# Kernel optimization log

Hardware: AMD Instinct MI355X
Metric: run time of the kernel (lower is better)

## Reference

```python
import jax, jax.numpy as jnp
import numpy as np

CRACK_VAL = 0.05  # intensity written along crack lines


def _crack_mask(endpoints, H, W):
    """Vectorized Bresenham rasterization.
    endpoints: [B, K, 4] int32 rows (y0, x0, y1, x1).
    Returns bool mask [B, 1, H, W] of pixels covered by any crack line.
    """
    B, K, _ = endpoints.shape
    ep = endpoints.reshape(-1, 4).astype(jnp.int32)  # [N=B*K, 4]
    y0, x0, y1, x1 = ep[:, 0], ep[:, 1], ep[:, 2], ep[:, 3]
    dx = jnp.abs(x1 - x0)
    dy = jnp.abs(y1 - y0)
    sx = jnp.where(x0 < x1, 1, -1).astype(jnp.int32)
    sy = jnp.where(y0 < y1, 1, -1).astype(jnp.int32)
    nsteps = jnp.maximum(dx, dy)  # line has nsteps+1 pixels
    T = max(H, W)  # static upper bound on line length

    def step(carry, t):
        cx, cy, err = carry
        valid = t <= nsteps  # pixel emitted this step is on the line
        rec = (cx, cy, valid)
        e2 = 2 * err
        cond_x = e2 > -dy
        cond_y = e2 < dx
        err = err - jnp.where(cond_x, dy, 0) + jnp.where(cond_y, dx, 0)
        cx = cx + jnp.where(cond_x, sx, 0)
        cy = cy + jnp.where(cond_y, sy, 0)
        return (cx, cy, err), rec

    init = (x0, y0, dx - dy)
    _, (cxs, cys, valids) = jax.lax.scan(step, init, jnp.arange(T, dtype=jnp.int32))
    # cxs/cys/valids: [T, N]
    bidx = jnp.broadcast_to(jnp.arange(B * K, dtype=jnp.int32) // K, cxs.shape)
    inb = (cys >= 0) & (cys < H) & (cxs >= 0) & (cxs < W)  # matches original bounds check
    ok = valids & inb
    flat = bidx * (H * W) + jnp.clip(cys, 0, H - 1) * W + jnp.clip(cxs, 0, W - 1)
    mask = jnp.zeros(B * H * W, dtype=bool).at[flat.ravel()].max(ok.ravel())
    return mask.reshape(B, 1, H, W)


def setup_inputs() -> dict:
    key = jax.random.key(0)
    k1, k2 = jax.random.split(key)
    B, C, H, W = 16, 3, 1024, 1024
    n_cracks = 8
    x = jax.random.uniform(k1, (B, C, H, W), dtype=jnp.float32)
    endpoints = jax.random.randint(k2, (B, n_cracks, 4), 0, H, dtype=jnp.int32)
    return {"x": x, "endpoints": endpoints}


def reference(x, endpoints):
    B, C, H, W = x.shape
    mask = _crack_mask(endpoints, H, W)  # [B,1,H,W], broadcasts over C
    out = jnp.where(mask, jnp.asarray(CRACK_VAL, x.dtype), x)
    return jnp.clip(out, 0.0, 1.0)
```

## Files before the change

### kernel.cpp

```cpp
#include <hip/hip_runtime.h>

#define CRACK_VAL 0.05f

__global__ void __launch_bounds__(256) lenscrack_clamp_copy(
    const float4* __restrict__ in, float4* __restrict__ out, int n4) {
    int i = blockIdx.x * blockDim.x + threadIdx.x;
    if (i < n4) {
        float4 v = in[i];
        v.x = fminf(fmaxf(v.x, 0.0f), 1.0f);
        v.y = fminf(fmaxf(v.y, 0.0f), 1.0f);
        v.z = fminf(fmaxf(v.z, 0.0f), 1.0f);
        v.w = fminf(fmaxf(v.w, 0.0f), 1.0f);
        out[i] = v;
    }
}

#define MAXT 1024

__global__ void __launch_bounds__(256) lenscrack_raster(
    const int* __restrict__ ep, float* __restrict__ out,
    int K, int C, int H, int W) {
    __shared__ int offs[MAXT];

    for (int t = threadIdx.x; t < MAXT; t += 256) offs[t] = -1;
    __syncthreads();

    int line = blockIdx.x;
    int b = line / K;

    if (threadIdx.x == 0) {
        const int* e = ep + (size_t)line * 4;
        int y0 = e[0], x0 = e[1], y1 = e[2], x1 = e[3];
        int dx = abs(x1 - x0);
        int dy = abs(y1 - y0);
        int sx = (x0 < x1) ? 1 : -1;
        int sy = (y0 < y1) ? 1 : -1;
        int nsteps = max(dx, dy);

        int x = x0, y = y0, err = dx - dy;
        for (int t = 0; t <= nsteps; ++t) {
            if (x >= 0 && x < W && y >= 0 && y < H)
                offs[t] = y * W + x;
            int e2 = 2 * err;
            bool cx = (e2 > -dy);
            bool cy = (e2 < dx);
            if (cx) { err -= dy; x += sx; }
            if (cy) { err += dx; y += sy; }
        }
    }
    __syncthreads();

    size_t HW = (size_t)H * W;
    float* base = out + (size_t)b * C * HW;
    for (int i = threadIdx.x; i < C * MAXT; i += 256) {
        int t = i & (MAXT - 1);
        int c = i >> 10;
        int o = offs[t];
        if (o >= 0) base[(size_t)c * HW + o] = CRACK_VAL;
    }
}

extern "C" void kernel_launch(void* const* d_in, const int* in_sizes, int n_in,
                              void* d_out, int out_size, void* d_ws, size_t ws_size,
                              hipStream_t stream) {
    const float* x  = (const float*)d_in[0];
    const int*   ep = (const int*)d_in[1];
    float* out = (float*)d_out;

    const int B = 16, C = 3, H = 1024, W = 1024, K = 8;

    int n4 = out_size / 4;
    int block = 256;
    int grid = (n4 + block - 1) / block;
    lenscrack_clamp_copy<<<grid, block, 0, stream>>>(
        (const float4*)x, (float4*)out, n4);

    lenscrack_raster<<<B * K, 256, 0, stream>>>(ep, out, K, C, H, W);
}
```

Measured before the change: 395.1 us.

## Rasterize crack lines in parallel with closed-form per-pixel Bresenham coordinates

```diff
diff --git a/kernel.cpp b/kernel.cpp
--- a/kernel.cpp
+++ b/kernel.cpp
@@ -15,48 +15,35 @@
     }
 }
 
-#define MAXT 1024
-
 __global__ void __launch_bounds__(256) lenscrack_raster(
     const int* __restrict__ ep, float* __restrict__ out,
     int K, int C, int H, int W) {
-    __shared__ int offs[MAXT];
+    int line = blockIdx.x >> 2;
+    int t    = ((blockIdx.x & 3) << 8) | threadIdx.x;
 
-    for (int t = threadIdx.x; t < MAXT; t += 256) offs[t] = -1;
-    __syncthreads();
+    const int* e = ep + (size_t)line * 4;
+    int y0 = e[0], x0 = e[1], y1 = e[2], x1 = e[3];
+    int dx = abs(x1 - x0);
+    int dy = abs(y1 - y0);
+    int sx = (x0 < x1) ? 1 : -1;
+    int sy = (y0 < y1) ? 1 : -1;
+    int dmaj = max(dx, dy);
+    if (t > dmaj) return;
 
-    int line = blockIdx.x;
-    int b = line / K;
+    int dmin = min(dx, dy);
+    int minor = (dmaj > 0) ? (2 * t * dmin + dmaj - 1) / (2 * dmaj) : 0;
 
-    if (threadIdx.x == 0) {
-        const int* e = ep + (size_t)line * 4;
-        int y0 = e[0], x0 = e[1], y1 = e[2], x1 = e[3];
-        int dx = abs(x1 - x0);
-        int dy = abs(y1 - y0);
-        int sx = (x0 < x1) ? 1 : -1;
-        int sy = (y0 < y1) ? 1 : -1;
-        int nsteps = max(dx, dy);
+    bool xmaj = (dx >= dy);
+    int x = x0 + sx * (xmaj ? t : minor);
+    int y = y0 + sy * (xmaj ? minor : t);
 
-        int x = x0, y = y0, err = dx - dy;
-        for (int t = 0; t <= nsteps; ++t) {
-            if (x >= 0 && x < W && y >= 0 && y < H)
-                offs[t] = y * W + x;
-            int e2 = 2 * err;
-            bool cx = (e2 > -dy);
-            bool cy = (e2 < dx);
-            if (cx) { err -= dy; x += sx; }
-            if (cy) { err += dx; y += sy; }
-        }
-    }
-    __syncthreads();
-
-    size_t HW = (size_t)H * W;
-    float* base = out + (size_t)b * C * HW;
-    for (int i = threadIdx.x; i < C * MAXT; i += 256) {
-        int t = i & (MAXT - 1);
-        int c = i >> 10;
-        int o = offs[t];
-        if (o >= 0) base[(size_t)c * HW + o] = CRACK_VAL;
+    if (x >= 0 && x < W && y >= 0 && y < H) {
+        int b = line / K;
+        size_t HW = (size_t)H * W;
+        float* base = out + (size_t)b * C * HW + (size_t)y * W + (size_t)x;
+        base[0]      = CRACK_VAL;
+        base[HW]     = CRACK_VAL;
+        base[2 * HW] = CRACK_VAL;
     }
 }
 
@@ -75,5 +62,5 @@
     lenscrack_clamp_copy<<<grid, block, 0, stream>>>(
         (const float4*)x, (float4*)out, n4);
 
-    lenscrack_raster<<<B * K, 256, 0, stream>>>(ep, out, K, C, H, W);
+    lenscrack_raster<<<B * K * 4, 256, 0, stream>>>(ep, out, K, C, H, W);
 }
```

Result: faster. 328.2 us (-16.9%).
